# Performance work log

Hardware: AMD Instinct MI355X
Metric: run time of the kernel (lower is better)

## Reference

```python
import jax, jax.numpy as jnp
import numpy as np

P_TOP = 0.1          # fraction of brightest pixels for atmosphere
LEC_K = 3            # local-extremum conv kernel size (w=3 in forward)
HID = 64             # hidden channels of stand-in Net


def _conv2d(x, w, pad):
    return jax.lax.conv_general_dilated(
        x, w, window_strides=(1, 1), padding=[(pad, pad), (pad, pad)],
        dimension_numbers=("NCHW", "OIHW", "NCHW"))


def _lec_weights(k, dtype):
    # LocalExtremumConv.init_weights: all +/-1/k^2 with +/-1 at the center
    base = jnp.full((1, 1, k, k), 1.0 / (k * k), dtype=dtype)
    base = base.at[0, 0, k // 2, k // 2].set(1.0)
    return -base, base  # (min_weights, max_weights)


def setup_inputs() -> dict:
    key = jax.random.key(0)
    ks = jax.random.split(key, 8)
    B, C, H, W = 8, 3, 512, 512
    x = jax.random.uniform(ks[0], (B, C, H, W), dtype=jnp.float32)
    s1 = 1.0 / np.sqrt(C * 9)
    s2 = 1.0 / np.sqrt(HID * 9)
    return {
        "x": x,
        "net_w1": jax.random.normal(ks[1], (HID, C, 3, 3), jnp.float32) * s1,
        "net_b1": jnp.zeros((HID,), jnp.float32),
        "net_w2": jax.random.normal(ks[2], (C, HID, 3, 3), jnp.float32) * s2,
        "net_b2": jnp.zeros((C,), jnp.float32),
        "color_w": jax.random.normal(ks[3], (3, 3), jnp.float32) * (1.0 / np.sqrt(3)),
        "color_b": jnp.zeros((3,), jnp.float32),
        "conv_w": jax.random.normal(ks[4], (4, 3, 1, 1), jnp.float32) * (1.0 / np.sqrt(3)),
        "conv_b": jnp.zeros((4,), jnp.float32),
    }


def reference(x, net_w1, net_b1, net_w2, net_b2, color_w, color_b, conv_w, conv_b):
    B, C, H, W = x.shape
    # --- stand-in Net: 3->64->3 conv enhancement, sigmoid output ---
    h = jax.nn.relu(_conv2d(x, net_w1, 1) + net_b1[None, :, None, None])
    img_high = jax.nn.sigmoid(_conv2d(h, net_w2, 1) + net_b2[None, :, None, None])
    # --- stand-in Color_pred: GAP -> linear -> sigmoid -> (B,3,1,1) gain ---
    color = jax.nn.sigmoid(x.mean(axis=(2, 3)) @ color_w.T + color_b)
    img_high = img_high * color[:, :, None, None]
    # --- 1x1 conv -> split K (1ch), Bias (3ch); residual correction ---
    feat = _conv2d(img_high, conv_w, 0) + conv_b[None, :, None, None]
    K, Bt = feat[:, 0:1], feat[:, 1:4]
    x_out = K * x - Bt + x
    # --- illumination channel: reflect pad + channel min/max + LEC convs ---
    pad = LEC_K // 2
    xp = jnp.pad(x_out, ((0, 0), (0, 0), (pad, pad), (pad, pad)), mode="reflect")
    x_max = xp.max(axis=1, keepdims=True)
    _, max_w = _lec_weights(LEC_K, x.dtype)
    bright = jax.nn.relu(_conv2d(x_max, max_w, 0))  # (B,1,H,W)
    # --- atmosphere: top-p% brightest pixels, gather + mean ---
    # NOTE: faithful to torch images.view(B,-1,C) on NCHW (layout-scrambled)
    flat_img = x_out.reshape(B, H * W, C)
    flat_bright = bright.reshape(B, H * W)
    num_pixels = int(P_TOP * H * W)
    _, idx = jax.lax.top_k(flat_bright, num_pixels)          # (B, num_pixels)
    picked = jnp.take_along_axis(flat_img, idx[:, :, None], axis=1)
    A = picked.mean(axis=1)                                   # (B, C)
    return (x_out, A)
```

## Files before the change

kernel.cpp:

```cpp
#include <hip/hip_runtime.h>
#include <hip/hip_bf16.h>

#define Hn 512
#define Wn 512
#define HWn (512 * 512)
#define KTOP 26214

typedef __attribute__((ext_vector_type(8))) short frag_ab;
typedef __attribute__((ext_vector_type(4))) float frag_cd;

__device__ __forceinline__ float sigf(float z) { return 1.0f / (1.0f + __expf(-z)); }

__device__ __forceinline__ short f2bf(float f) {
  unsigned u = __float_as_uint(f);
  u += 0x7FFFu + ((u >> 16) & 1u);
  return (short)(u >> 16);
}

__device__ __forceinline__ unsigned aload(const unsigned* p) {
  return __hip_atomic_load(p, __ATOMIC_RELAXED, __HIP_MEMORY_SCOPE_AGENT);
}

__global__ __launch_bounds__(256) void k_means(
    const float* __restrict__ x, float* __restrict__ means, unsigned* __restrict__ doneCnt,
    const float* __restrict__ w1, const float* __restrict__ b1, const float* __restrict__ w2,
    const float* __restrict__ cw, const float* __restrict__ cb,
    short* __restrict__ w1A, short* __restrict__ w2A, float* __restrict__ colorG)
{
  const int tid = threadIdx.x;
  __shared__ int lastS;
  int bc = blockIdx.x >> 5;
  int slice = blockIdx.x & 31;
  const float4* p = (const float4*)(x + bc * HWn + slice * 8192);
  float s = 0.f;
  for (int i = tid; i < 2048; i += 256) { float4 v = p[i]; s += v.x + v.y + v.z + v.w; }
  for (int off = 32; off > 0; off >>= 1) s += __shfl_down(s, off);
  if ((tid & 63) == 0) atomicAdd(&means[bc], s);
  __syncthreads();
  if (tid == 0) {
    unsigned tk = __hip_atomic_fetch_add(doneCnt, 1u, __ATOMIC_RELAXED, __HIP_MEMORY_SCOPE_AGENT);
    lastS = (tk == 767);
  }
  __syncthreads();
  if (!lastS) return;

  {
    int chunk = tid >> 6, lane = tid & 63;
    int m = lane & 15, q = lane >> 4;
    for (int j = 0; j < 8; ++j) {
      int k = q * 8 + j;
      float v = (k < 27) ? w1[(chunk * 16 + m) * 27 + k] : 0.f;
      w1A[tid * 8 + j] = f2bf(v);
    }
  }
  for (int i = tid; i < 384; i += 256) {
    int step = i >> 6, lane = i & 63;
    int m = lane & 15, q = lane >> 4;
    int dx = step >> 1, half = step & 1;
    int dy = m / 3, oc = m - dy * 3;
    for (int j = 0; j < 8; ++j) {
      int ch = half * 32 + q * 8 + j;
      float v = (m < 9) ? w2[oc * 576 + ch * 9 + dy * 3 + dx] : 0.f;
      w2A[i * 8 + j] = f2bf(v);
    }
  }
  if (tid < 24) {
    int b = tid / 3, oc = tid % 3;
    float z = cb[oc];
    for (int j = 0; j < 3; ++j)
      z += (atomicAdd(&means[b * 3 + j], 0.f) * (1.0f / (float)HWn)) * cw[oc * 3 + j];
    colorG[tid] = sigf(z);
  }
}

__global__ __launch_bounds__(256, 5) void k_fused(
    const float* __restrict__ x, const float* __restrict__ b1,
    const float* __restrict__ b2, const float* __restrict__ convw, const float* __restrict__ convb,
    const short* __restrict__ w1Ag, const short* __restrict__ w2Ag,
    const float* __restrict__ colorG, float* __restrict__ out)
{
  __shared__ __align__(16) unsigned short xs[720];
  __shared__ __align__(16) unsigned short hb[12960];
  __shared__ float bs[64];
  __shared__ float b2s[3], colorS[3], cwS[12], cbS[4];

  const int tid = threadIdx.x;
  const int wid = tid >> 6, lane = tid & 63;
  const int n = lane & 15, q = lane >> 4;
  const int tx0 = blockIdx.x * 16, ty0 = blockIdx.y * 8;
  const int b = blockIdx.z;

  if (tid < 180) {
    int c = tid / 60, rem = tid - c * 60;
    int yy = rem / 5, xq = (rem - yy * 5) * 4;
    int gy = ty0 - 2 + yy, gx0 = tx0 - 2 + xq;
    bool rowok = (unsigned)gy < 512u;
    const float* rp = x + (b * 3 + c) * HWn + (gy << 9) + gx0;
    float v0 = (rowok && (unsigned)(gx0 + 0) < 512u) ? rp[0] : 0.f;
    float v1 = (rowok && (unsigned)(gx0 + 1) < 512u) ? rp[1] : 0.f;
    float v2 = (rowok && (unsigned)(gx0 + 2) < 512u) ? rp[2] : 0.f;
    float v3 = (rowok && (unsigned)(gx0 + 3) < 512u) ? rp[3] : 0.f;
    __hip_bfloat162 c01 = __float22bfloat162_rn(make_float2(v0, v1));
    __hip_bfloat162 c23 = __float22bfloat162_rn(make_float2(v2, v3));
    uint2 v2w; v2w.x = *(unsigned*)&c01; v2w.y = *(unsigned*)&c23;
    *(uint2*)(xs + c * 240 + yy * 20 + xq) = v2w;
  }
  if (tid < 64) bs[tid] = b1[tid];
  if (tid < 3)  b2s[tid] = b2[tid];
  if (tid < 3)  colorS[tid] = colorG[b * 3 + tid];
  if (tid < 12) cwS[tid] = convw[tid];
  if (tid < 4)  cbS[tid] = convb[tid];

  frag_ab w1f[4];
#pragma unroll
  for (int ck = 0; ck < 4; ++ck) w1f[ck] = *(const frag_ab*)(w1Ag + (ck * 64 + lane) * 8);

  int kb[8];
#pragma unroll
  for (int j = 0; j < 8; ++j) {
    int k = q * 8 + j;
    int kk = (k < 27) ? k : (k - 27);
    int ic = kk / 9; int r = kk - ic * 9;
    kb[j] = (ic * 240 + (r / 3) * 20 + (r % 3)) * 2;
  }
  __syncthreads();

  float biasr[4][4];
#pragma unroll
  for (int ck = 0; ck < 4; ++ck)
#pragma unroll
    for (int r = 0; r < 4; ++r) biasr[ck][r] = bs[ck * 16 + q * 4 + r];

  for (int g = wid; g < 12; g += 4) {
    int pt = g * 16 + n;
    bool ptok = pt < 180;
    int ptc = ptok ? pt : 0;
    int pty = (ptc * 3641) >> 16;
    int ptx = ptc - pty * 18;
    int baseB = (pty * 20 + ptx) * 2;
    int gy = ty0 - 1 + pty, gx = tx0 - 1 + ptx;
    bool valid = ptok && (unsigned)gy < 512u && (unsigned)gx < 512u;
    frag_ab B;
#pragma unroll
    for (int j = 0; j < 8; ++j)
      B[j] = *(const short*)((const char*)xs + baseB + kb[j]);
#pragma unroll
    for (int ck = 0; ck < 4; ++ck) {
      frag_cd D = {biasr[ck][0], biasr[ck][1], biasr[ck][2], biasr[ck][3]};
      D = __builtin_amdgcn_mfma_f32_16x16x32_bf16(w1f[ck], B, D, 0, 0, 0);
      if (ptok) {
        float2 p01 = make_float2(fmaxf(D[0], 0.f), fmaxf(D[1], 0.f));
        float2 p23 = make_float2(fmaxf(D[2], 0.f), fmaxf(D[3], 0.f));
        __hip_bfloat162 c01 = __float22bfloat162_rn(p01);
        __hip_bfloat162 c23 = __float22bfloat162_rn(p23);
        unsigned lo = valid ? *(unsigned*)&c01 : 0u;
        unsigned hi = valid ? *(unsigned*)&c23 : 0u;
        uint2 v2; v2.x = lo; v2.y = hi;
        *(uint2*)(hb + pt * 72 + ck * 16 + q * 4) = v2;
      }
    }
  }

  frag_ab w2f[6];
#pragma unroll
  for (int i = 0; i < 6; ++i) w2f[i] = *(const frag_ab*)(w2Ag + (i * 64 + lane) * 8);
  __syncthreads();

  for (int r = wid; r < 10; r += 4) {
    frag_cd acc = {0.f, 0.f, 0.f, 0.f};
#pragma unroll
    for (int i = 0; i < 6; ++i) {
      int dx = i >> 1;
      int chb = (i & 1) * 64 + q * 16;
      frag_ab Bf = *(const frag_ab*)((const char*)hb + (r * 18 + n + dx) * 144 + chb);
      acc = __builtin_amdgcn_mfma_f32_16x16x32_bf16(w2f[i], Bf, acc, 0, 0, 0);
    }
    float* dp = (float*)(hb + r * 1296) + n * 10 + q * 4;
    if (q < 2) {
      *(float2*)dp = make_float2(acc[0], acc[1]);
      *(float2*)(dp + 2) = make_float2(acc[2], acc[3]);
    } else if (q == 2) {
      dp[0] = acc[0];
    }
  }
  __syncthreads();

  if (tid < 128) {
    int y = tid >> 4, xcol = tid & 15;
    float a0 = b2s[0], a1 = b2s[1], a2 = b2s[2];
#pragma unroll
    for (int dy = 0; dy < 3; ++dy) {
      const float* dp = (const float*)(hb + (y + dy) * 1296) + xcol * 10 + dy * 3;
      a0 += dp[0]; a1 += dp[1]; a2 += dp[2];
    }
    float ih0 = colorS[0] * sigf(a0);
    float ih1 = colorS[1] * sigf(a1);
    float ih2 = colorS[2] * sigf(a2);
    float Kv = cwS[0] * ih0 + cwS[1]  * ih1 + cwS[2]  * ih2 + cbS[0];
    float f1 = cwS[3] * ih0 + cwS[4]  * ih1 + cwS[5]  * ih2 + cbS[1];
    float f2 = cwS[6] * ih0 + cwS[7]  * ih1 + cwS[8]  * ih2 + cbS[2];
    float f3 = cwS[9] * ih0 + cwS[10] * ih1 + cwS[11] * ih2 + cbS[3];
    float xc0 = __bfloat162float(*(const __hip_bfloat16*)&xs[0 * 240 + (y + 2) * 20 + (xcol + 2)]);
    float xc1 = __bfloat162float(*(const __hip_bfloat16*)&xs[1 * 240 + (y + 2) * 20 + (xcol + 2)]);
    float xc2 = __bfloat162float(*(const __hip_bfloat16*)&xs[2 * 240 + (y + 2) * 20 + (xcol + 2)]);
    int oi = ((ty0 + y) << 9) + (tx0 + xcol);
    out[(b * 3 + 0) * HWn + oi] = Kv * xc0 - f1 + xc0;
    out[(b * 3 + 1) * HWn + oi] = Kv * xc1 - f2 + xc1;
    out[(b * 3 + 2) * HWn + oi] = Kv * xc2 - f3 + xc2;
  }
}

__device__ __forceinline__ void softBarrier(unsigned* ctr, unsigned target) {
  __syncthreads();
  if (threadIdx.x == 0) {
    __hip_atomic_fetch_add(ctr, 1u, __ATOMIC_RELAXED, __HIP_MEMORY_SCOPE_AGENT);
    while (__hip_atomic_load(ctr, __ATOMIC_RELAXED, __HIP_MEMORY_SCOPE_AGENT) < target)
      __builtin_amdgcn_s_sleep(2);
  }
  __syncthreads();
}

__device__ void sel256(const unsigned* __restrict__ h, unsigned kneed,
                       unsigned* sm, unsigned* oBin, unsigned* oAbove)
{
  const int t = threadIdx.x;
  sm[t] = aload(&h[t]);
  __syncthreads();
  for (int d = 1; d < 256; d <<= 1) {
    unsigned add = (t + d < 256) ? sm[t + d] : 0u;
    __syncthreads();
    sm[t] += add;
    __syncthreads();
  }
  unsigned mine = sm[t];
  unsigned nxt = (t < 255) ? sm[t + 1] : 0u;
  if (mine >= kneed && nxt < kneed) { *oBin = (unsigned)t; *oAbove = nxt; }
  __syncthreads();
}

__device__ void sel4096(const unsigned* __restrict__ h, unsigned kneed,
                        unsigned* sm, unsigned* oBin, unsigned* oAbove)
{
  const int t = threadIdx.x;
  unsigned loc[16]; unsigned sum = 0;
#pragma unroll
  for (int i = 0; i < 16; ++i) { loc[i] = aload(&h[t * 16 + i]); sum += loc[i]; }
  sm[t] = sum;
  __syncthreads();
  for (int d = 1; d < 256; d <<= 1) {
    unsigned add = (t + d < 256) ? sm[t + d] : 0u;
    __syncthreads();
    sm[t] += add;
    __syncthreads();
  }
  unsigned mine = sm[t];
  unsigned nxt = (t < 255) ? sm[t + 1] : 0u;
  if (mine >= kneed && nxt < kneed) {
    unsigned acc = nxt;
    for (int i = 15; i >= 0; --i) {
      unsigned c = loc[i];
      if (acc + c >= kneed) { *oBin = (unsigned)(t * 16 + i); *oAbove = acc; break; }
      acc += c;
    }
  }
  __syncthreads();
}

__global__ __launch_bounds__(256) void k_tail(
    const float* __restrict__ outv,
    unsigned* __restrict__ h1, unsigned* __restrict__ h12,
    unsigned* __restrict__ eqTaken, float* __restrict__ Asum,
    unsigned* __restrict__ barCtr, unsigned* __restrict__ doneCnt, float* __restrict__ outA)
{
  __shared__ __align__(16) char smem[17408];
  __shared__ __align__(16) float brightS[2048];
  __shared__ unsigned sB1, sA1, sB2, sA2;
  __shared__ float red[4][3];
  __shared__ int lastA;

  float (*xm)[516] = (float (*)[516])smem;
  unsigned* hh = (unsigned*)smem;
  unsigned* sm = (unsigned*)(smem + 16384);

  const int tid = threadIdx.x;
  const int b = blockIdx.x >> 7, strip = blockIdx.x & 127;
  const int y0 = strip * 4;
  const float* op = outv + b * 3 * HWn;
  unsigned* bar = barCtr + b * 48;

  for (int idx = tid; idx < 768; idx += 256) {
    int r = idx >> 7, seg = idx & 127;
    int gy = y0 - 1 + r; gy = (gy < 0) ? -gy : (gy > 511 ? 1022 - gy : gy);
    int c0 = seg * 4;
    const float* rp = op + (gy << 9) + c0;
    float4 v0 = *(const float4*)rp;
    float4 v1 = *(const float4*)(rp + HWn);
    float4 v2 = *(const float4*)(rp + 2 * HWn);
    xm[r][c0 + 1] = fmaxf(v0.x, fmaxf(v1.x, v2.x));
    xm[r][c0 + 2] = fmaxf(v0.y, fmaxf(v1.y, v2.y));
    xm[r][c0 + 3] = fmaxf(v0.z, fmaxf(v1.z, v2.z));
    xm[r][c0 + 4] = fmaxf(v0.w, fmaxf(v1.w, v2.w));
  }
  if (tid < 12) {
    int r = tid >> 1, side = tid & 1;
    int gy = y0 - 1 + r; gy = (gy < 0) ? -gy : (gy > 511 ? 1022 - gy : gy);
    int gx = side ? 510 : 1;
    float m = fmaxf(op[(gy << 9) + gx], fmaxf(op[HWn + (gy << 9) + gx], op[2 * HWn + (gy << 9) + gx]));
    xm[r][side ? 513 : 0] = m;
  }
  __syncthreads();
  {
    const int row = tid >> 6, cl = tid & 63;
#pragma unroll 4
    for (int i = 0; i < 8; ++i) {
      int c = cl + (i << 6);
      float s0 = xm[row][c]     + xm[row][c + 1]     + xm[row][c + 2];
      float s1 = xm[row + 1][c] + xm[row + 1][c + 1] + xm[row + 1][c + 2];
      float s2 = xm[row + 2][c] + xm[row + 2][c + 1] + xm[row + 2][c + 2];
      float s = (s0 + s1 + s2) * (1.f / 9.f) + xm[row + 1][c + 1] * (8.f / 9.f);
      s = fmaxf(s, 0.f);
      brightS[(row << 9) + c] = s;
    }
  }
  __syncthreads();

  hh[tid] = 0;
  __syncthreads();
  {
    unsigned cb0 = 0x100, cc0 = 0, cb1 = 0x100, cc1 = 0;
    const float4* bp4 = (const float4*)brightS;
#pragma unroll
    for (int it = 0; it < 2; ++it) {
      float4 v = bp4[it * 256 + tid];
      unsigned bins[4] = { __float_as_uint(v.x) >> 24, __float_as_uint(v.y) >> 24,
                           __float_as_uint(v.z) >> 24, __float_as_uint(v.w) >> 24 };
#pragma unroll
      for (int j = 0; j < 4; ++j) {
        unsigned bb = bins[j];
        if (bb == cb0) ++cc0;
        else if (bb == cb1) ++cc1;
        else if (!cc0) { cb0 = bb; cc0 = 1; }
        else if (!cc1) { cb1 = bb; cc1 = 1; }
        else atomicAdd(&hh[bb], 1u);
      }
    }
    if (cc0) atomicAdd(&hh[cb0], cc0);
    if (cc1) atomicAdd(&hh[cb1], cc1);
  }
  __syncthreads();
  if (hh[tid]) atomicAdd(&h1[(b << 8) + tid], hh[tid]);
  softBarrier(bar, 128);

  sel256(h1 + (b << 8), KTOP, sm, &sB1, &sA1);
  for (int i = tid; i < 4096; i += 256) hh[i] = 0;
  __syncthreads();
  const float4* bp = (const float4*)brightS;
  const unsigned sb1 = sB1;
#pragma unroll
  for (int it = 0; it < 2; ++it) {
    float4 v = bp[it * 256 + tid];
    unsigned u0 = __float_as_uint(v.x), u1 = __float_as_uint(v.y);
    unsigned u2 = __float_as_uint(v.z), u3 = __float_as_uint(v.w);
    if ((u0 >> 24) == sb1) atomicAdd(&hh[(u0 >> 12) & 0xFFFu], 1u);
    if ((u1 >> 24) == sb1) atomicAdd(&hh[(u1 >> 12) & 0xFFFu], 1u);
    if ((u2 >> 24) == sb1) atomicAdd(&hh[(u2 >> 12) & 0xFFFu], 1u);
    if ((u3 >> 24) == sb1) atomicAdd(&hh[(u3 >> 12) & 0xFFFu], 1u);
  }
  __syncthreads();
  for (int i = tid; i < 4096; i += 256)
    if (hh[i]) atomicAdd(&h12[(b << 12) + i], hh[i]);
  if (tid == 0) { sB2 = 0xFFFu; sA2 = 0u; }
  softBarrier(bar + 16, 128);

  sel4096(h12 + (b << 12), KTOP - sA1, sm, &sB2, &sA2);
  const unsigned T20 = (sB1 << 12) | sB2;
  const unsigned ne = KTOP - sA1 - sA2;
  float v0 = 0.f, v1 = 0.f, v2 = 0.f;
  for (int it = 0; it < 8; ++it) {
    int li = it * 256 + tid;
    int pix = (y0 << 9) + li;
    unsigned u20 = __float_as_uint(brightS[li]) >> 12;
    bool take = u20 > T20;
    if (u20 == T20) {
      if (aload(&eqTaken[b * 16]) < ne) {
        unsigned old = atomicAdd(&eqTaken[b * 16], 1u);
        take = old < ne;
      }
    }
    if (take) {
      v0 += op[3 * pix];
      v1 += op[3 * pix + 1];
      v2 += op[3 * pix + 2];
    }
  }
  for (int off = 32; off > 0; off >>= 1) {
    v0 += __shfl_down(v0, off);
    v1 += __shfl_down(v1, off);
    v2 += __shfl_down(v2, off);
  }
  int w = tid >> 6;
  if ((tid & 63) == 0) { red[w][0] = v0; red[w][1] = v1; red[w][2] = v2; }
  __syncthreads();
  if (tid == 0) {
    atomicAdd(&Asum[b * 3 + 0], red[0][0] + red[1][0] + red[2][0] + red[3][0]);
    atomicAdd(&Asum[b * 3 + 1], red[0][1] + red[1][1] + red[2][1] + red[3][1]);
    atomicAdd(&Asum[b * 3 + 2], red[0][2] + red[1][2] + red[2][2] + red[3][2]);
  }
  __syncthreads();
  if (tid == 0) {
    unsigned tk = __hip_atomic_fetch_add(doneCnt, 1u, __ATOMIC_RELAXED, __HIP_MEMORY_SCOPE_AGENT);
    lastA = (tk == 1023);
  }
  __syncthreads();
  if (lastA && tid < 24)
    outA[3 * HWn * 8 + tid] = atomicAdd(&Asum[tid], 0.f) * (1.0f / (float)KTOP);
}

extern "C" void kernel_launch(void* const* d_in, const int* in_sizes, int n_in,
                              void* d_out, int out_size, void* d_ws, size_t ws_size,
                              hipStream_t stream)
{
  const float* x     = (const float*)d_in[0];
  const float* w1    = (const float*)d_in[1];
  const float* b1    = (const float*)d_in[2];
  const float* w2    = (const float*)d_in[3];
  const float* b2    = (const float*)d_in[4];
  const float* cw    = (const float*)d_in[5];
  const float* cb    = (const float*)d_in[6];
  const float* convw = (const float*)d_in[7];
  const float* convb = (const float*)d_in[8];
  float* out = (float*)d_out;
  char* ws = (char*)d_ws;

  unsigned* h1        = (unsigned*)(ws + 8388608);
  unsigned* h12       = (unsigned*)(ws + 8396800);
  float*    Asum      = (float*)(ws + 8658944);
  unsigned* eqTaken   = (unsigned*)(ws + 8659040);
  float*    means     = (float*)(ws + 8659552);
  unsigned* meansDone = (unsigned*)(ws + 8659648);
  unsigned* accumDone = (unsigned*)(ws + 8659680);
  unsigned* barCtr    = (unsigned*)(ws + 8659712);
  short*    w1Ag      = (short*)(ws + 8661248);
  short*    w2Ag      = (short*)(ws + 8665344);
  float*    colorG    = (float*)(ws + 8683776);

  hipMemsetAsync(ws + 8388608, 0, 8661248 - 8388608, stream);

  k_means<<<768, 256, 0, stream>>>(x, means, meansDone, w1, b1, w2, cw, cb, w1Ag, w2Ag, colorG);
  k_fused<<<dim3(32, 64, 8), 256, 0, stream>>>(x, b1, b2, convw, convb, w1Ag, w2Ag, colorG, out);
  k_tail<<<1024, 256, 0, stream>>>(out, h1, h12, eqTaken, Asum, barCtr, accumDone, out);
}
```

Measured before the change: 281.7 us.

## Precompute channel max in fused kernel and halve tail grid with taller strips

The fused kernel now writes a per-pixel channel-max plane to workspace, so the tail kernel reads one plane instead of three channels when building the bright map. The tail kernel also processes 8-row strips with 512 blocks instead of 4-row strips with 1024 blocks, which cuts halo re-reads and softBarrier participants per batch. The cost is an extra 8 MB write in the fused kernel and larger shared memory per tail block.

```diff
diff --git a/kernel.cpp b/kernel.cpp
--- a/kernel.cpp
+++ b/kernel.cpp
@@ -77,7 +77,7 @@
     const float* __restrict__ x, const float* __restrict__ b1,
     const float* __restrict__ b2, const float* __restrict__ convw, const float* __restrict__ convb,
     const short* __restrict__ w1Ag, const short* __restrict__ w2Ag,
-    const float* __restrict__ colorG, float* __restrict__ out)
+    const float* __restrict__ colorG, float* __restrict__ out, float* __restrict__ Mb)
 {
   __shared__ __align__(16) unsigned short xs[720];
   __shared__ __align__(16) unsigned short hb[12960];
@@ -204,9 +204,13 @@
     float xc1 = __bfloat162float(*(const __hip_bfloat16*)&xs[1 * 240 + (y + 2) * 20 + (xcol + 2)]);
     float xc2 = __bfloat162float(*(const __hip_bfloat16*)&xs[2 * 240 + (y + 2) * 20 + (xcol + 2)]);
     int oi = ((ty0 + y) << 9) + (tx0 + xcol);
-    out[(b * 3 + 0) * HWn + oi] = Kv * xc0 - f1 + xc0;
-    out[(b * 3 + 1) * HWn + oi] = Kv * xc1 - f2 + xc1;
-    out[(b * 3 + 2) * HWn + oi] = Kv * xc2 - f3 + xc2;
+    float o0 = Kv * xc0 - f1 + xc0;
+    float o1 = Kv * xc1 - f2 + xc1;
+    float o2 = Kv * xc2 - f3 + xc2;
+    out[(b * 3 + 0) * HWn + oi] = o0;
+    out[(b * 3 + 1) * HWn + oi] = o1;
+    out[(b * 3 + 2) * HWn + oi] = o2;
+    Mb[b * HWn + oi] = fmaxf(fmaxf(o0, o1), o2);
   }
 }
 
@@ -267,13 +271,13 @@
 }
 
 __global__ __launch_bounds__(256) void k_tail(
-    const float* __restrict__ outv,
+    const float* __restrict__ Mbuf, const float* __restrict__ outv,
     unsigned* __restrict__ h1, unsigned* __restrict__ h12,
     unsigned* __restrict__ eqTaken, float* __restrict__ Asum,
     unsigned* __restrict__ barCtr, unsigned* __restrict__ doneCnt, float* __restrict__ outA)
 {
-  __shared__ __align__(16) char smem[17408];
-  __shared__ __align__(16) float brightS[2048];
+  __shared__ __align__(16) char smem[20640];
+  __shared__ __align__(16) float brightS[4096];
   __shared__ unsigned sB1, sA1, sB2, sA2;
   __shared__ float red[4][3];
   __shared__ int lastA;
@@ -283,37 +287,34 @@
   unsigned* sm = (unsigned*)(smem + 16384);
 
   const int tid = threadIdx.x;
-  const int b = blockIdx.x >> 7, strip = blockIdx.x & 127;
-  const int y0 = strip * 4;
+  const int b = blockIdx.x >> 6, strip = blockIdx.x & 63;
+  const int y0 = strip * 8;
+  const float* mp = Mbuf + b * HWn;
   const float* op = outv + b * 3 * HWn;
   unsigned* bar = barCtr + b * 48;
 
-  for (int idx = tid; idx < 768; idx += 256) {
+  for (int idx = tid; idx < 1280; idx += 256) {
     int r = idx >> 7, seg = idx & 127;
     int gy = y0 - 1 + r; gy = (gy < 0) ? -gy : (gy > 511 ? 1022 - gy : gy);
     int c0 = seg * 4;
-    const float* rp = op + (gy << 9) + c0;
-    float4 v0 = *(const float4*)rp;
-    float4 v1 = *(const float4*)(rp + HWn);
-    float4 v2 = *(const float4*)(rp + 2 * HWn);
-    xm[r][c0 + 1] = fmaxf(v0.x, fmaxf(v1.x, v2.x));
-    xm[r][c0 + 2] = fmaxf(v0.y, fmaxf(v1.y, v2.y));
-    xm[r][c0 + 3] = fmaxf(v0.z, fmaxf(v1.z, v2.z));
-    xm[r][c0 + 4] = fmaxf(v0.w, fmaxf(v1.w, v2.w));
-  }
-  if (tid < 12) {
+    float4 v = *(const float4*)(mp + (gy << 9) + c0);
+    xm[r][c0 + 1] = v.x;
+    xm[r][c0 + 2] = v.y;
+    xm[r][c0 + 3] = v.z;
+    xm[r][c0 + 4] = v.w;
+  }
+  if (tid < 20) {
     int r = tid >> 1, side = tid & 1;
     int gy = y0 - 1 + r; gy = (gy < 0) ? -gy : (gy > 511 ? 1022 - gy : gy);
     int gx = side ? 510 : 1;
-    float m = fmaxf(op[(gy << 9) + gx], fmaxf(op[HWn + (gy << 9) + gx], op[2 * HWn + (gy << 9) + gx]));
-    xm[r][side ? 513 : 0] = m;
+    xm[r][side ? 513 : 0] = mp[(gy << 9) + gx];
   }
   __syncthreads();
   {
-    const int row = tid >> 6, cl = tid & 63;
+    const int row = tid >> 5, cl = tid & 31;
 #pragma unroll 4
-    for (int i = 0; i < 8; ++i) {
-      int c = cl + (i << 6);
+    for (int i = 0; i < 16; ++i) {
+      int c = cl + (i << 5);
       float s0 = xm[row][c]     + xm[row][c + 1]     + xm[row][c + 2];
       float s1 = xm[row + 1][c] + xm[row + 1][c + 1] + xm[row + 1][c + 2];
       float s2 = xm[row + 2][c] + xm[row + 2][c + 1] + xm[row + 2][c + 2];
@@ -330,7 +331,7 @@
     unsigned cb0 = 0x100, cc0 = 0, cb1 = 0x100, cc1 = 0;
     const float4* bp4 = (const float4*)brightS;
 #pragma unroll
-    for (int it = 0; it < 2; ++it) {
+    for (int it = 0; it < 4; ++it) {
       float4 v = bp4[it * 256 + tid];
       unsigned bins[4] = { __float_as_uint(v.x) >> 24, __float_as_uint(v.y) >> 24,
                            __float_as_uint(v.z) >> 24, __float_as_uint(v.w) >> 24 };
@@ -349,7 +350,7 @@
   }
   __syncthreads();
   if (hh[tid]) atomicAdd(&h1[(b << 8) + tid], hh[tid]);
-  softBarrier(bar, 128);
+  softBarrier(bar, 64);
 
   sel256(h1 + (b << 8), KTOP, sm, &sB1, &sA1);
   for (int i = tid; i < 4096; i += 256) hh[i] = 0;
@@ -357,7 +358,7 @@
   const float4* bp = (const float4*)brightS;
   const unsigned sb1 = sB1;
 #pragma unroll
-  for (int it = 0; it < 2; ++it) {
+  for (int it = 0; it < 4; ++it) {
     float4 v = bp[it * 256 + tid];
     unsigned u0 = __float_as_uint(v.x), u1 = __float_as_uint(v.y);
     unsigned u2 = __float_as_uint(v.z), u3 = __float_as_uint(v.w);
@@ -370,13 +371,13 @@
   for (int i = tid; i < 4096; i += 256)
     if (hh[i]) atomicAdd(&h12[(b << 12) + i], hh[i]);
   if (tid == 0) { sB2 = 0xFFFu; sA2 = 0u; }
-  softBarrier(bar + 16, 128);
+  softBarrier(bar + 16, 64);
 
   sel4096(h12 + (b << 12), KTOP - sA1, sm, &sB2, &sA2);
   const unsigned T20 = (sB1 << 12) | sB2;
   const unsigned ne = KTOP - sA1 - sA2;
   float v0 = 0.f, v1 = 0.f, v2 = 0.f;
-  for (int it = 0; it < 8; ++it) {
+  for (int it = 0; it < 16; ++it) {
     int li = it * 256 + tid;
     int pix = (y0 << 9) + li;
     unsigned u20 = __float_as_uint(brightS[li]) >> 12;
@@ -409,7 +410,7 @@
   __syncthreads();
   if (tid == 0) {
     unsigned tk = __hip_atomic_fetch_add(doneCnt, 1u, __ATOMIC_RELAXED, __HIP_MEMORY_SCOPE_AGENT);
-    lastA = (tk == 1023);
+    lastA = (tk == 511);
   }
   __syncthreads();
   if (lastA && tid < 24)
@@ -432,6 +433,7 @@
   float* out = (float*)d_out;
   char* ws = (char*)d_ws;
 
+  float*    Mbuf      = (float*)(ws);
   unsigned* h1        = (unsigned*)(ws + 8388608);
   unsigned* h12       = (unsigned*)(ws + 8396800);
   float*    Asum      = (float*)(ws + 8658944);
@@ -447,6 +449,6 @@
   hipMemsetAsync(ws + 8388608, 0, 8661248 - 8388608, stream);
 
   k_means<<<768, 256, 0, stream>>>(x, means, meansDone, w1, b1, w2, cw, cb, w1Ag, w2Ag, colorG);
-  k_fused<<<dim3(32, 64, 8), 256, 0, stream>>>(x, b1, b2, convw, convb, w1Ag, w2Ag, colorG, out);
-  k_tail<<<1024, 256, 0, stream>>>(out, h1, h12, eqTaken, Asum, barCtr, accumDone, out);
-}
+  k_fused<<<dim3(32, 64, 8), 256, 0, stream>>>(x, b1, b2, convw, convb, w1Ag, w2Ag, colorG, out, Mbuf);
+  k_tail<<<512, 256, 0, stream>>>(Mbuf, out, h1, h12, eqTaken, Asum, barCtr, accumDone, out);
+}
```

Result: faster. 252.7 us (-10.3%).
